# Kernel optimization log

Measured on AMD Instinct MI355X. Metric: run time of the kernel, lower is better.

The kernel has to match this reference:

```python
import jax, jax.numpy as jnp
import numpy as np

EMBED_DIM = 1024
NUM_HEADS = 16
HEAD_DIM = EMBED_DIM // NUM_HEADS
B, T = 4, 2048


def setup_inputs() -> dict:
    key = jax.random.key(0)
    k1, k2, k3, k4, k5 = jax.random.split(key, 5)
    s = 0.02
    return {
        "x": jax.random.normal(k1, (B, T, EMBED_DIM), dtype=jnp.float32),
        "w_qkv": jax.random.normal(k2, (EMBED_DIM, 3 * EMBED_DIM), dtype=jnp.float32) * s,
        "b_qkv": jnp.zeros((3 * EMBED_DIM,), dtype=jnp.float32),
        "w_proj": jax.random.normal(k3, (EMBED_DIM, EMBED_DIM), dtype=jnp.float32) * s,
        "b_proj": jnp.zeros((EMBED_DIM,), dtype=jnp.float32),
    }


def reference(x, w_qkv, b_qkv, w_proj, b_proj):
    Bx, Tx, C = x.shape
    H, D = NUM_HEADS, HEAD_DIM
    qkv = x @ w_qkv + b_qkv                      # [B,T,3C]
    qkv = qkv.reshape(Bx, Tx, 3, H, D)
    q = qkv[:, :, 0].transpose(0, 2, 1, 3)       # [B,H,T,D]
    k = qkv[:, :, 1].transpose(0, 2, 1, 3)
    v = qkv[:, :, 2].transpose(0, 2, 1, 3)
    scale = 1.0 / jnp.sqrt(jnp.asarray(D, dtype=x.dtype))
    att = jnp.einsum("bhqd,bhkd->bhqk", q, k) * scale   # [B,H,T,T]
    causal = jnp.tril(jnp.ones((Tx, Tx), dtype=bool))
    att = jnp.where(causal[None, None], att, jnp.asarray(-jnp.inf, dtype=att.dtype))
    att = jax.nn.softmax(att, axis=-1)
    y = jnp.einsum("bhqk,bhkd->bhqd", att, v)            # [B,H,T,D]
    y = y.transpose(0, 2, 1, 3).reshape(Bx, Tx, C)
    return y @ w_proj + b_proj
```

## Files before the change

### kernel.cpp

```cpp
#include <hip/hip_runtime.h>
#include <hip/hip_bf16.h>

typedef __bf16 bf16_t;
typedef __attribute__((ext_vector_type(4))) __bf16 bf16x4;
typedef __attribute__((ext_vector_type(8))) __bf16 bf16x8;
typedef __attribute__((ext_vector_type(4))) float f32x4;
typedef __attribute__((ext_vector_type(16))) float f32x16;
typedef __attribute__((ext_vector_type(4))) unsigned int uint4v;

__device__ __forceinline__ void async_copy16(const void* g, void* lds) {
  __builtin_amdgcn_global_load_lds(
      (const __attribute__((address_space(1))) unsigned int*)g,
      (__attribute__((address_space(3))) unsigned int*)lds, 16, 0, 0);
}

__device__ __forceinline__ unsigned pkbf(float lo, float hi) {
  unsigned short a = __builtin_bit_cast(unsigned short, (bf16_t)lo);
  unsigned short b = __builtin_bit_cast(unsigned short, (bf16_t)hi);
  return (unsigned)a | ((unsigned)b << 16);
}

__device__ __forceinline__ float swap_add(float v) {
  return v + __shfl_xor(v, 32);
}

__global__ __launch_bounds__(256) void cast_f32_bf16(
    const float* __restrict__ in, bf16_t* __restrict__ out, long n8) {
  long i = (long)blockIdx.x * blockDim.x + threadIdx.x;
  if (i >= n8) return;
  const float4* p = (const float4*)(in + i * 8);
  float4 a = p[0], b = p[1];
  bf16x8 o;
  o[0] = (bf16_t)a.x; o[1] = (bf16_t)a.y; o[2] = (bf16_t)a.z; o[3] = (bf16_t)a.w;
  o[4] = (bf16_t)b.x; o[5] = (bf16_t)b.y; o[6] = (bf16_t)b.z; o[7] = (bf16_t)b.w;
  *(bf16x8*)(out + i * 8) = o;
}

__global__ __launch_bounds__(256) void transpose_cast(
    const float* __restrict__ in, bf16_t* __restrict__ out, int R, int C) {
  __shared__ float tile[32][33];
  int r0 = blockIdx.y * 32, c0 = blockIdx.x * 32;
  int tx = threadIdx.x, ty = threadIdx.y;
#pragma unroll
  for (int j = 0; j < 32; j += 8)
    tile[ty + j][tx] = in[(size_t)(r0 + ty + j) * C + c0 + tx];
  __syncthreads();
#pragma unroll
  for (int j = 0; j < 32; j += 8)
    out[(size_t)(c0 + ty + j) * R + r0 + tx] = (bf16_t)tile[tx][ty + j];
}

template <int MODE>
__global__ __launch_bounds__(256) void gemm_bf16(
    const bf16_t* __restrict__ A, const bf16_t* __restrict__ Bt,
    const float* __restrict__ bias, int M, int N, int K,
    bf16_t* __restrict__ Qo, bf16_t* __restrict__ Ko, bf16_t* __restrict__ Vo,
    float* __restrict__ Fo) {
  constexpr int BK = 64;
  __shared__ bf16_t As[128 * BK];
  __shared__ bf16_t Bs[128 * BK];
  const int tid = threadIdx.x;
  const int wid = tid >> 6, lane = tid & 63;
  const int wr = wid >> 1, wc = wid & 1;
  const int g = lane >> 4, c = lane & 15;
  const int m0 = blockIdx.y * 128, n0 = blockIdx.x * 128;
  const int lrow = lane >> 3;
  const int lseg = lane & 7;

  f32x4 acc[4][4] = {};

  for (int kt = 0; kt < K; kt += BK) {
#pragma unroll
    for (int cc = 0; cc < 4; ++cc) {
      int chunk = cc * 4 + wid;
      int row = chunk * 8 + lrow;
      int seg = lseg ^ (row & 7);
      async_copy16(A + (size_t)(m0 + row) * K + kt + seg * 8, &As[chunk * 512]);
    }
#pragma unroll
    for (int cc = 0; cc < 4; ++cc) {
      int chunk = cc * 4 + wid;
      int row = chunk * 8 + lrow;
      int seg = lseg ^ (row & 7);
      async_copy16(Bt + (size_t)(n0 + row) * K + kt + seg * 8, &Bs[chunk * 512]);
    }
    __syncthreads();
#pragma unroll
    for (int ks = 0; ks < 2; ++ks) {
      bf16x8 af[4], bfr[4];
#pragma unroll
      for (int m = 0; m < 4; ++m) {
        int row = wr * 64 + m * 16 + c;
        int seg = (ks * 4 + g) ^ (row & 7);
        af[m] = *(const bf16x8*)&As[row * 64 + seg * 8];
      }
#pragma unroll
      for (int n = 0; n < 4; ++n) {
        int row = wc * 64 + n * 16 + c;
        int seg = (ks * 4 + g) ^ (row & 7);
        bfr[n] = *(const bf16x8*)&Bs[row * 64 + seg * 8];
      }
#pragma unroll
      for (int m = 0; m < 4; ++m)
#pragma unroll
        for (int n = 0; n < 4; ++n)
          acc[m][n] =
              __builtin_amdgcn_mfma_f32_16x16x32_bf16(af[m], bfr[n], acc[m][n], 0, 0, 0);
    }
    __syncthreads();
  }

  if (MODE == 1) {
#pragma unroll
    for (int m = 0; m < 4; ++m) {
      int grow = m0 + wr * 64 + m * 16 + g * 4;
#pragma unroll
      for (int n = 0; n < 4; ++n) {
        int gcol = n0 + wc * 64 + n * 16 + c;
        float bs = bias[gcol];
#pragma unroll
        for (int i = 0; i < 4; ++i)
          Fo[(size_t)(grow + i) * N + gcol] = acc[m][n][i] + bs;
      }
    }
  } else {
    constexpr float QSC = 0.125f * 1.44269504088896f;
#pragma unroll
    for (int m = 0; m < 4; ++m) {
      int grow = m0 + wr * 64 + m * 16 + g * 4;
#pragma unroll
      for (int n = 0; n < 4; ++n) {
        int gcol = n0 + wc * 64 + n * 16 + c;
        float bs = bias[gcol];
        int sel = gcol >> 10;
        int h = (gcol >> 6) & 15;
        int d = gcol & 63;
        if (sel < 2) {
          bf16_t* dst = (sel == 0) ? Qo : Ko;
          float scl = (sel == 0) ? QSC : 1.0f;
#pragma unroll
          for (int i = 0; i < 4; ++i) {
            int row = grow + i;
            int b = row >> 11, t = row & 2047;
            dst[(((size_t)(b * 16 + h)) * 2048 + t) * 64 + d] =
                (bf16_t)((acc[m][n][i] + bs) * scl);
          }
        } else {
          int b = grow >> 11, t = grow & 2047;
          bf16x4 v;
#pragma unroll
          for (int i = 0; i < 4; ++i) v[i] = (bf16_t)(acc[m][n][i] + bs);
          *(bf16x4*)&Vo[(((size_t)(b * 16 + h)) * 64 + d) * 2048 + t] = v;
        }
      }
    }
  }
}

__global__ __launch_bounds__(256, 4) void attn_fwd(
    const bf16_t* __restrict__ Qg_, const bf16_t* __restrict__ Kg_,
    const bf16_t* __restrict__ Vtg_, bf16_t* __restrict__ Y) {
  __shared__ bf16_t Ks[2][64 * 64];
  __shared__ bf16_t Vs[2][64 * 64];
  const int tid = threadIdx.x, wid = tid >> 6, lane = tid & 63;
  const int l31 = lane & 31, hi = lane >> 5;
  const int bh = blockIdx.x;
  const int b = bh >> 4, h = bh & 15;
  const bf16_t* Qg = Qg_ + (size_t)bh * 2048 * 64;
  const bf16_t* Kg = Kg_ + (size_t)bh * 2048 * 64;
  const bf16_t* Vtg = Vtg_ + (size_t)bh * 64 * 2048;

  const int qt = 15 - blockIdx.y;
  const int q0 = qt * 128;
  const int qw = q0 + wid * 32 + l31;
  const int qmaxw = q0 + wid * 32 + 31;
  const int NT = 2 * qt + 2;

  bf16x8 qf[4];
#pragma unroll
  for (int ks = 0; ks < 4; ++ks)
    qf[ks] = *(const bf16x8*)&Qg[(size_t)qw * 64 + ks * 16 + hi * 8];

  f32x4 sa = {};
  f32x16 ot0 = {}, ot1 = {};

#pragma unroll
  for (int cc = 0; cc < 2; ++cc) {
    int chunk = wid * 2 + cc;
    int row = chunk * 8 + (lane >> 3);
    int seg = (lane & 7) ^ (row & 7);
    async_copy16(Kg + (size_t)row * 64 + seg * 8, &Ks[0][chunk * 512]);
    async_copy16(Vtg + (size_t)row * 2048 + seg * 8, &Vs[0][chunk * 512]);
  }
  __syncthreads();

  for (int kt = 0; kt < NT; ++kt) {
    const int buf = kt & 1;
    if (kt + 1 < NT) {
#pragma unroll
      for (int cc = 0; cc < 2; ++cc) {
        int chunk = wid * 2 + cc;
        int row = chunk * 8 + (lane >> 3);
        int seg = (lane & 7) ^ (row & 7);
        async_copy16(Kg + (size_t)((kt + 1) * 64 + row) * 64 + seg * 8,
                     &Ks[buf ^ 1][chunk * 512]);
        async_copy16(Vtg + (size_t)row * 2048 + (kt + 1) * 64 + seg * 8,
                     &Vs[buf ^ 1][chunk * 512]);
      }
    }
    const int kv0 = kt * 64;
    if (kv0 <= qmaxw) {
      f32x16 st0 = {}, st1 = {};
      __builtin_amdgcn_s_setprio(1);
#pragma unroll
      for (int ks = 0; ks < 4; ++ks) {
        int segb = ks * 2 + hi;
        {
          int row = l31;
          bf16x8 kf = *(const bf16x8*)&Ks[buf][row * 64 + (segb ^ (row & 7)) * 8];
          st0 = __builtin_amdgcn_mfma_f32_32x32x16_bf16(kf, qf[ks], st0, 0, 0, 0);
        }
        {
          int row = 32 + l31;
          bf16x8 kf = *(const bf16x8*)&Ks[buf][row * 64 + (segb ^ (row & 7)) * 8];
          st1 = __builtin_amdgcn_mfma_f32_32x32x16_bf16(kf, qf[ks], st1, 0, 0, 0);
        }
      }
      __builtin_amdgcn_s_setprio(0);
      if (kv0 + 63 > qw) {
#pragma unroll
        for (int r = 0; r < 16; ++r) {
          int kvl = (r & 3) + 8 * (r >> 2) + 4 * hi;
          if (kv0 + kvl > qw) st0[r] = -1e30f;
          if (kv0 + 32 + kvl > qw) st1[r] = -1e30f;
        }
      }
#pragma unroll
      for (int r = 0; r < 16; ++r) {
        st0[r] = exp2f(st0[r]);
        st1[r] = exp2f(st1[r]);
      }
#pragma unroll
      for (int r = 0; r < 4; ++r)
        sa[r] += ((st0[r] + st0[r + 4]) + (st0[r + 8] + st0[r + 12])) +
                 ((st1[r] + st1[r + 4]) + (st1[r + 8] + st1[r + 12]));
      bf16x8 pb[4];
#pragma unroll
      for (int nt = 0; nt < 2; ++nt) {
#pragma unroll
        for (int s = 0; s < 2; ++s) {
          float p0 = nt ? st1[8 * s + 0] : st0[8 * s + 0];
          float p1 = nt ? st1[8 * s + 1] : st0[8 * s + 1];
          float p2 = nt ? st1[8 * s + 2] : st0[8 * s + 2];
          float p3 = nt ? st1[8 * s + 3] : st0[8 * s + 3];
          float p4 = nt ? st1[8 * s + 4] : st0[8 * s + 4];
          float p5 = nt ? st1[8 * s + 5] : st0[8 * s + 5];
          float p6 = nt ? st1[8 * s + 6] : st0[8 * s + 6];
          float p7 = nt ? st1[8 * s + 7] : st0[8 * s + 7];
          unsigned a0 = pkbf(p0, p1), a1 = pkbf(p2, p3);
          unsigned b0 = pkbf(p4, p5), b1 = pkbf(p6, p7);
          unsigned t0 = (unsigned)__shfl_xor((int)(hi ? a0 : b0), 32);
          unsigned t1 = (unsigned)__shfl_xor((int)(hi ? a1 : b1), 32);
          uint4v words;
          words[0] = hi ? t0 : a0;
          words[1] = hi ? t1 : a1;
          words[2] = hi ? b0 : t0;
          words[3] = hi ? b1 : t1;
          pb[nt * 2 + s] = __builtin_bit_cast(bf16x8, words);
        }
      }
      __builtin_amdgcn_s_setprio(1);
#pragma unroll
      for (int ks2 = 0; ks2 < 4; ++ks2) {
        int segb = ks2 * 2 + hi;
        {
          int row = l31;
          bf16x8 vf = *(const bf16x8*)&Vs[buf][row * 64 + (segb ^ (row & 7)) * 8];
          ot0 = __builtin_amdgcn_mfma_f32_32x32x16_bf16(vf, pb[ks2], ot0, 0, 0, 0);
        }
        {
          int row = 32 + l31;
          bf16x8 vf = *(const bf16x8*)&Vs[buf][row * 64 + (segb ^ (row & 7)) * 8];
          ot1 = __builtin_amdgcn_mfma_f32_32x32x16_bf16(vf, pb[ks2], ot1, 0, 0, 0);
        }
      }
      __builtin_amdgcn_s_setprio(0);
    }
    __syncthreads();
  }

  float l = swap_add((sa[0] + sa[1]) + (sa[2] + sa[3]));
  float inv = 1.0f / l;
  size_t yrow = ((size_t)b * 2048 + qw) * 1024 + h * 64;
#pragma unroll
  for (int rq = 0; rq < 4; ++rq) {
    int dbase = 8 * rq + 4 * hi;
    bf16x4 v0, v1;
#pragma unroll
    for (int j = 0; j < 4; ++j) {
      v0[j] = (bf16_t)(ot0[rq * 4 + j] * inv);
      v1[j] = (bf16_t)(ot1[rq * 4 + j] * inv);
    }
    *(bf16x4*)&Y[yrow + dbase] = v0;
    *(bf16x4*)&Y[yrow + 32 + dbase] = v1;
  }
}

extern "C" void kernel_launch(void* const* d_in, const int* in_sizes, int n_in,
                              void* d_out, int out_size, void* d_ws, size_t ws_size,
                              hipStream_t stream) {
  (void)in_sizes; (void)n_in; (void)out_size; (void)ws_size;
  const float* x = (const float*)d_in[0];
  const float* w_qkv = (const float*)d_in[1];
  const float* b_qkv = (const float*)d_in[2];
  const float* w_proj = (const float*)d_in[3];
  const float* b_proj = (const float*)d_in[4];
  float* out = (float*)d_out;

  char* ws = (char*)d_ws;
  size_t off = 0;
  bf16_t* xb = (bf16_t*)(ws + off); off += (size_t)8192 * 1024 * 2;
  bf16_t* wqkvT = (bf16_t*)(ws + off); off += (size_t)3072 * 1024 * 2;
  bf16_t* wprojT = (bf16_t*)(ws + off); off += (size_t)1024 * 1024 * 2;
  bf16_t* Qb = (bf16_t*)(ws + off); off += (size_t)8192 * 1024 * 2;
  bf16_t* Kb = (bf16_t*)(ws + off); off += (size_t)8192 * 1024 * 2;
  bf16_t* Vtb = (bf16_t*)(ws + off); off += (size_t)8192 * 1024 * 2;
  bf16_t* Yb = xb;

  cast_f32_bf16<<<4096, 256, 0, stream>>>(x, xb, (long)8192 * 1024 / 8);
  transpose_cast<<<dim3(96, 32), dim3(32, 8), 0, stream>>>(w_qkv, wqkvT, 1024, 3072);
  transpose_cast<<<dim3(32, 32), dim3(32, 8), 0, stream>>>(w_proj, wprojT, 1024, 1024);
  gemm_bf16<0><<<dim3(24, 64), 256, 0, stream>>>(xb, wqkvT, b_qkv, 8192, 3072, 1024,
                                                 Qb, Kb, Vtb, nullptr);
  attn_fwd<<<dim3(64, 16), 256, 0, stream>>>(Qb, Kb, Vtb, Yb);
  gemm_bf16<1><<<dim3(8, 64), 256, 0, stream>>>(Yb, wprojT, b_proj, 8192, 1024, 1024,
                                                nullptr, nullptr, nullptr, out);
}
```

Baseline: 182.1 us.

## Triple-buffer GEMM loads with async copies and enlarge tiles to 256x128

Replaces the single-buffered bf16 GEMM with a three-stage pipeline that issues async global-to-LDS copies two k-tiles ahead, syncing via explicit vmcnt waits and raw barriers instead of __syncthreads. The block grows to 512 threads (8 waves) covering a 256x128 output tile, and MFMA sections are wrapped in raised wave priority. The goal is to hide global memory latency behind compute and get more reuse of the B tile. In exchange it uses much more LDS (triple buffers of larger tiles, 144 KB per block), which limits occupancy. The hand-written waitcnt values must also match the per-thread count of copies issued per stage.

Measured after the change: 194.1 us. 1.07x slower.

```diff
diff --git a/kernel.cpp b/kernel.cpp
--- a/kernel.cpp
+++ b/kernel.cpp
@@ -51,40 +51,61 @@
 }
 
 template <int MODE>
-__global__ __launch_bounds__(256) void gemm_bf16(
+__global__ __launch_bounds__(512, 2) void gemm_pipe(
     const bf16_t* __restrict__ A, const bf16_t* __restrict__ Bt,
     const float* __restrict__ bias, int M, int N, int K,
     bf16_t* __restrict__ Qo, bf16_t* __restrict__ Ko, bf16_t* __restrict__ Vo,
     float* __restrict__ Fo) {
-  constexpr int BK = 64;
-  __shared__ bf16_t As[128 * BK];
-  __shared__ bf16_t Bs[128 * BK];
+  __shared__ bf16_t As[3][256 * 64];
+  __shared__ bf16_t Bs[3][128 * 64];
   const int tid = threadIdx.x;
   const int wid = tid >> 6, lane = tid & 63;
   const int wr = wid >> 1, wc = wid & 1;
   const int g = lane >> 4, c = lane & 15;
-  const int m0 = blockIdx.y * 128, n0 = blockIdx.x * 128;
-  const int lrow = lane >> 3;
-  const int lseg = lane & 7;
+  const int m0 = blockIdx.y * 256, n0 = blockIdx.x * 128;
+  const int srow = tid >> 3;
+  const int sseg = tid & 7;
 
   f32x4 acc[4][4] = {};
-
-  for (int kt = 0; kt < K; kt += BK) {
-#pragma unroll
-    for (int cc = 0; cc < 4; ++cc) {
-      int chunk = cc * 4 + wid;
-      int row = chunk * 8 + lrow;
-      int seg = lseg ^ (row & 7);
-      async_copy16(A + (size_t)(m0 + row) * K + kt + seg * 8, &As[chunk * 512]);
-    }
-#pragma unroll
-    for (int cc = 0; cc < 4; ++cc) {
-      int chunk = cc * 4 + wid;
-      int row = chunk * 8 + lrow;
-      int seg = lseg ^ (row & 7);
-      async_copy16(Bt + (size_t)(n0 + row) * K + kt + seg * 8, &Bs[chunk * 512]);
-    }
-    __syncthreads();
+  const int NT = K >> 6;
+
+  const bf16_t* Abase = A + (size_t)m0 * K;
+  const bf16_t* Bbase = Bt + (size_t)n0 * K;
+
+#define STAGE(BUF, T)                                                          \
+  {                                                                            \
+    const bf16_t* Ab_ = Abase + (T)*64;                                        \
+    const bf16_t* Bb_ = Bbase + (T)*64;                                        \
+    _Pragma("unroll") for (int cc = 0; cc < 4; ++cc) {                         \
+      int row = cc * 64 + srow;                                                \
+      int seg = sseg ^ (row & 7);                                              \
+      async_copy16(Ab_ + (size_t)row * K + seg * 8,                            \
+                   &As[BUF][cc * 4096 + wid * 512]);                           \
+    }                                                                          \
+    _Pragma("unroll") for (int cc = 0; cc < 2; ++cc) {                         \
+      int row = cc * 64 + srow;                                                \
+      int seg = sseg ^ (row & 7);                                              \
+      async_copy16(Bb_ + (size_t)row * K + seg * 8,                            \
+                   &Bs[BUF][cc * 4096 + wid * 512]);                           \
+    }                                                                          \
+  }
+
+  STAGE(0, 0);
+  STAGE(1, 1);
+
+  for (int t = 0; t < NT; ++t) {
+    const int buf = t % 3;
+    if (t + 1 < NT)
+      asm volatile("s_waitcnt vmcnt(6)" ::: "memory");
+    else
+      asm volatile("s_waitcnt vmcnt(0)" ::: "memory");
+    asm volatile("s_barrier" ::: "memory");
+    if (t + 2 < NT) {
+      const int nbuf = (t + 2) % 3;
+      STAGE(nbuf, t + 2);
+    }
+    const bf16_t* Ab = &As[buf][0];
+    const bf16_t* Bb = &Bs[buf][0];
 #pragma unroll
     for (int ks = 0; ks < 2; ++ks) {
       bf16x8 af[4], bfr[4];
@@ -92,23 +113,25 @@
       for (int m = 0; m < 4; ++m) {
         int row = wr * 64 + m * 16 + c;
         int seg = (ks * 4 + g) ^ (row & 7);
-        af[m] = *(const bf16x8*)&As[row * 64 + seg * 8];
+        af[m] = *(const bf16x8*)&Ab[row * 64 + seg * 8];
       }
 #pragma unroll
       for (int n = 0; n < 4; ++n) {
         int row = wc * 64 + n * 16 + c;
         int seg = (ks * 4 + g) ^ (row & 7);
-        bfr[n] = *(const bf16x8*)&Bs[row * 64 + seg * 8];
-      }
+        bfr[n] = *(const bf16x8*)&Bb[row * 64 + seg * 8];
+      }
+      __builtin_amdgcn_s_setprio(1);
 #pragma unroll
       for (int m = 0; m < 4; ++m)
 #pragma unroll
         for (int n = 0; n < 4; ++n)
           acc[m][n] =
               __builtin_amdgcn_mfma_f32_16x16x32_bf16(af[m], bfr[n], acc[m][n], 0, 0, 0);
-    }
-    __syncthreads();
-  }
+      __builtin_amdgcn_s_setprio(0);
+    }
+  }
+#undef STAGE
 
   if (MODE == 1) {
 #pragma unroll
@@ -330,9 +353,9 @@
   cast_f32_bf16<<<4096, 256, 0, stream>>>(x, xb, (long)8192 * 1024 / 8);
   transpose_cast<<<dim3(96, 32), dim3(32, 8), 0, stream>>>(w_qkv, wqkvT, 1024, 3072);
   transpose_cast<<<dim3(32, 32), dim3(32, 8), 0, stream>>>(w_proj, wprojT, 1024, 1024);
-  gemm_bf16<0><<<dim3(24, 64), 256, 0, stream>>>(xb, wqkvT, b_qkv, 8192, 3072, 1024,
+  gemm_pipe<0><<<dim3(24, 32), 512, 0, stream>>>(xb, wqkvT, b_qkv, 8192, 3072, 1024,
                                                  Qb, Kb, Vtb, nullptr);
   attn_fwd<<<dim3(64, 16), 256, 0, stream>>>(Qb, Kb, Vtb, Yb);
-  gemm_bf16<1><<<dim3(8, 64), 256, 0, stream>>>(Yb, wprojT, b_proj, 8192, 1024, 1024,
+  gemm_pipe<1><<<dim3(8, 32), 512, 0, stream>>>(Yb, wprojT, b_proj, 8192, 1024, 1024,
                                                 nullptr, nullptr, nullptr, out);
 }
```

## Double-buffer GEMM LDS tiles and swizzle workgroup order

Applied to the files above, without the earlier changes.

Converts both GEMMs to a two-stage LDS pipeline: the next K-tile is fetched asynchronously into the alternate buffer while MFMAs run on the current one, which removes one barrier per iteration. It also remaps workgroup IDs with a stride-8 swizzle to change which tiles run together, aiming for better L2 reuse across XCDs, and sets launch bounds to ask for two workgroups per CU. Shared memory use doubles to 64KB per block, which may limit occupancy. The single barrier per iteration also relies on the async loads completing before the next use, so there is a risk of a race on load completion.

Measured after the change: 179.8 us (median of 2 runs). About the same (-1.2%).

```diff
diff --git a/kernel.cpp b/kernel.cpp
--- a/kernel.cpp
+++ b/kernel.cpp
@@ -51,40 +51,52 @@
 }
 
 template <int MODE>
-__global__ __launch_bounds__(256) void gemm_bf16(
+__global__ __launch_bounds__(256, 2) void gemm_db(
     const bf16_t* __restrict__ A, const bf16_t* __restrict__ Bt,
     const float* __restrict__ bias, int M, int N, int K,
     bf16_t* __restrict__ Qo, bf16_t* __restrict__ Ko, bf16_t* __restrict__ Vo,
     float* __restrict__ Fo) {
   constexpr int BK = 64;
-  __shared__ bf16_t As[128 * BK];
-  __shared__ bf16_t Bs[128 * BK];
+  __shared__ bf16_t As[2][128 * BK];
+  __shared__ bf16_t Bs[2][128 * BK];
   const int tid = threadIdx.x;
   const int wid = tid >> 6, lane = tid & 63;
   const int wr = wid >> 1, wc = wid & 1;
   const int g = lane >> 4, c = lane & 15;
-  const int m0 = blockIdx.y * 128, n0 = blockIdx.x * 128;
+  const int nwg = gridDim.x * gridDim.y;
+  const int lid = blockIdx.y * gridDim.x + blockIdx.x;
+  const int swz = (lid & 7) * (nwg >> 3) + (lid >> 3);
+  const int m0 = (swz / gridDim.x) * 128, n0 = (swz % gridDim.x) * 128;
   const int lrow = lane >> 3;
   const int lseg = lane & 7;
 
   f32x4 acc[4][4] = {};
-
-  for (int kt = 0; kt < K; kt += BK) {
-#pragma unroll
-    for (int cc = 0; cc < 4; ++cc) {
-      int chunk = cc * 4 + wid;
-      int row = chunk * 8 + lrow;
-      int seg = lseg ^ (row & 7);
-      async_copy16(A + (size_t)(m0 + row) * K + kt + seg * 8, &As[chunk * 512]);
-    }
-#pragma unroll
-    for (int cc = 0; cc < 4; ++cc) {
-      int chunk = cc * 4 + wid;
-      int row = chunk * 8 + lrow;
-      int seg = lseg ^ (row & 7);
-      async_copy16(Bt + (size_t)(n0 + row) * K + kt + seg * 8, &Bs[chunk * 512]);
-    }
-    __syncthreads();
+  const int NT = K >> 6;
+
+#define STAGE(BUF, T)                                                         \
+  {                                                                           \
+    _Pragma("unroll") for (int cc = 0; cc < 4; ++cc) {                        \
+      int chunk = cc * 4 + wid;                                               \
+      int row = chunk * 8 + lrow;                                             \
+      int seg = lseg ^ (row & 7);                                             \
+      async_copy16(A + (size_t)(m0 + row) * K + (T)*BK + seg * 8,             \
+                   &As[BUF][chunk * 512]);                                    \
+    }                                                                         \
+    _Pragma("unroll") for (int cc = 0; cc < 4; ++cc) {                        \
+      int chunk = cc * 4 + wid;                                               \
+      int row = chunk * 8 + lrow;                                             \
+      int seg = lseg ^ (row & 7);                                             \
+      async_copy16(Bt + (size_t)(n0 + row) * K + (T)*BK + seg * 8,            \
+                   &Bs[BUF][chunk * 512]);                                    \
+    }                                                                         \
+  }
+
+  STAGE(0, 0);
+  __syncthreads();
+
+  for (int t = 0; t < NT; ++t) {
+    const int buf = t & 1;
+    if (t + 1 < NT) STAGE(buf ^ 1, t + 1);
 #pragma unroll
     for (int ks = 0; ks < 2; ++ks) {
       bf16x8 af[4], bfr[4];
@@ -92,13 +104,13 @@
       for (int m = 0; m < 4; ++m) {
         int row = wr * 64 + m * 16 + c;
         int seg = (ks * 4 + g) ^ (row & 7);
-        af[m] = *(const bf16x8*)&As[row * 64 + seg * 8];
+        af[m] = *(const bf16x8*)&As[buf][row * 64 + seg * 8];
       }
 #pragma unroll
       for (int n = 0; n < 4; ++n) {
         int row = wc * 64 + n * 16 + c;
         int seg = (ks * 4 + g) ^ (row & 7);
-        bfr[n] = *(const bf16x8*)&Bs[row * 64 + seg * 8];
+        bfr[n] = *(const bf16x8*)&Bs[buf][row * 64 + seg * 8];
       }
 #pragma unroll
       for (int m = 0; m < 4; ++m)
@@ -109,6 +121,7 @@
     }
     __syncthreads();
   }
+#undef STAGE
 
   if (MODE == 1) {
 #pragma unroll
@@ -330,9 +343,9 @@
   cast_f32_bf16<<<4096, 256, 0, stream>>>(x, xb, (long)8192 * 1024 / 8);
   transpose_cast<<<dim3(96, 32), dim3(32, 8), 0, stream>>>(w_qkv, wqkvT, 1024, 3072);
   transpose_cast<<<dim3(32, 32), dim3(32, 8), 0, stream>>>(w_proj, wprojT, 1024, 1024);
-  gemm_bf16<0><<<dim3(24, 64), 256, 0, stream>>>(xb, wqkvT, b_qkv, 8192, 3072, 1024,
-                                                 Qb, Kb, Vtb, nullptr);
+  gemm_db<0><<<dim3(24, 64), 256, 0, stream>>>(xb, wqkvT, b_qkv, 8192, 3072, 1024,
+                                               Qb, Kb, Vtb, nullptr);
   attn_fwd<<<dim3(64, 16), 256, 0, stream>>>(Qb, Kb, Vtb, Yb);
-  gemm_bf16<1><<<dim3(8, 64), 256, 0, stream>>>(Yb, wprojT, b_proj, 8192, 1024, 1024,
-                                                nullptr, nullptr, nullptr, out);
-}
+  gemm_db<1><<<dim3(8, 64), 256, 0, stream>>>(Yb, wprojT, b_proj, 8192, 1024, 1024,
+                                              nullptr, nullptr, nullptr, out);
+}
```
